# Kernel optimization log

Hardware: AMD Instinct MI355X
Metric: run time of the kernel (lower is better)

Reference implementation:

```python
import math
import jax, jax.numpy as jnp
import numpy as np

TOP_K = 2
_GELU_C = math.sqrt(2.0 / math.pi)

def gelu_new(x):
    # NewGELU: tanh approximation identical to the torch module
    return 0.5 * x * (1.0 + jnp.tanh(_GELU_C * (x + 0.044715 * x * x * x)))

def setup_inputs() -> dict:
    key = jax.random.key(0)
    ks = jax.random.split(key, 6)
    B, T, C, E, H = 2, 2048, 1024, 8, 4096
    s_in = 1.0 / math.sqrt(C)
    s_hid = 1.0 / math.sqrt(H)
    return {
        "x": jax.random.normal(ks[0], (B, T, C), dtype=jnp.float32),
        "router_w": jax.random.normal(ks[1], (E, C), dtype=jnp.float32) * s_in,
        "w_fc": jax.random.normal(ks[2], (E, C, H), dtype=jnp.float32) * s_in,
        "b_fc": jax.random.normal(ks[3], (E, H), dtype=jnp.float32) * 0.02,
        "w_proj": jax.random.normal(ks[4], (E, H, C), dtype=jnp.float32) * s_hid,
        "b_proj": jax.random.normal(ks[5], (E, C), dtype=jnp.float32) * 0.02,
    }

def reference(x, router_w, w_fc, b_fc, w_proj, b_proj):
    B, T, C = x.shape
    E = router_w.shape[0]
    N = B * T
    xf = x.reshape(N, C)
    # Router: Linear(C, E, bias=False), softmax, top-k, renormalize
    logits = xf @ router_w.T                              # [N, E]
    probs = jax.nn.softmax(logits, axis=-1)
    topk_probs, topk_idx = jax.lax.top_k(probs, TOP_K)    # [N, K]
    topk_probs = topk_probs / jnp.sum(topk_probs, axis=-1, keepdims=True)
    # Dense combine weights: zero for unselected experts -> same math as
    # gather/FFN/index_add over selected tokens (dropout=0).
    combine = jnp.zeros((N, E), dtype=x.dtype).at[
        jnp.arange(N)[:, None], topk_idx].add(topk_probs)  # [N, E]
    # Expert FFN applied per expert (batched GEMMs)
    h = gelu_new(jnp.einsum('nc,ech->neh', xf, w_fc) + b_fc)      # [N, E, H]
    out = jnp.einsum('neh,ehc->nec', h, w_proj) + b_proj          # [N, E, C]
    y = jnp.einsum('nec,ne->nc', out, combine)                    # [N, C]
    return y.reshape(B, T, C)
```

## Files before the change

kernel.cpp:

```cpp
#include <hip/hip_runtime.h>


#define NTOK  4096
#define CDIM  1024
#define HDIM  4096
#define NEXP  8
#define NPC   9216
#define MAXMT 72
#define KB_C  32
#define KB_H  128

typedef _Float16 half8 __attribute__((ext_vector_type(8)));
typedef float    f32x4 __attribute__((ext_vector_type(4)));

#define ASYNC_CP16(gp, lp)                                                         \
  __builtin_amdgcn_global_load_lds(                                                \
      (const __attribute__((address_space(1))) unsigned int*)(gp),                 \
      (__attribute__((address_space(3))) unsigned int*)(lp), 16, 0, 0)

#define BAR()     asm volatile("s_barrier" ::: "memory")
#define WAITVM4() asm volatile("s_waitcnt vmcnt(4)" ::: "memory")
#define WAITVM0() asm volatile("s_waitcnt vmcnt(0)" ::: "memory")

__device__ __forceinline__ float gelu_new(float x) {
    const float c = 0.7978845608028654f;
    return 0.5f * x * (1.0f + tanhf(c * (x + 0.044715f * x * x * x)));
}


__global__ void zero_u32(unsigned int* __restrict__ p, int n) {
    int i = blockIdx.x * 256 + threadIdx.x;
    if (i < n) p[i] = 0u;
}

__global__ void zero_meta(unsigned int* __restrict__ pt, unsigned int* __restrict__ pg,
                          unsigned int* __restrict__ cnt) {
    int i = blockIdx.x * 256 + threadIdx.x;
    if (i < NPC) { pt[i] = 0u; pg[i] = 0u; }
    if (i < NEXP) cnt[i] = 0u;
}


__global__ __launch_bounds__(256) void router_kernel(
    const float* __restrict__ x, const float* __restrict__ rw,
    int* __restrict__ tok_e, float* __restrict__ tok_w, int* __restrict__ counts)
{
    int wave = threadIdx.x >> 6, lane = threadIdx.x & 63;
    int n = blockIdx.x * 4 + wave;
    const float* xr = x + (size_t)n * CDIM;
    float acc[NEXP];
    #pragma unroll
    for (int e = 0; e < NEXP; ++e) acc[e] = 0.f;
    for (int c = lane; c < CDIM; c += 64) {
        float xv = xr[c];
        #pragma unroll
        for (int e = 0; e < NEXP; ++e) acc[e] = fmaf(xv, rw[e * CDIM + c], acc[e]);
    }
    #pragma unroll
    for (int e = 0; e < NEXP; ++e) {
        float v = acc[e];
        #pragma unroll
        for (int off = 32; off > 0; off >>= 1) v += __shfl_down(v, off);
        acc[e] = v;
    }
    if (lane == 0) {
        float l0 = -3.0e38f, l1 = -3.0e38f; int b0 = 0, b1 = 0;
        #pragma unroll
        for (int e = 0; e < NEXP; ++e) {
            float v = acc[e];
            if (v > l0)      { l1 = l0; b1 = b0; l0 = v; b0 = e; }
            else if (v > l1) { l1 = v; b1 = e; }
        }
        float t  = expf(l1 - l0);
        float w0 = 1.f / (1.f + t);
        float w1 = t  / (1.f + t);
        tok_e[n * 2]     = b0;  tok_e[n * 2 + 1] = b1;
        tok_w[n * 2]     = w0;  tok_w[n * 2 + 1] = w1;
        atomicAdd(&counts[b0], 1);
        atomicAdd(&counts[b1], 1);
    }
}

__global__ void plan_kernel(const int* __restrict__ counts, int* __restrict__ cursors,
                            int* __restrict__ mtiles, int* __restrict__ tile_expert)
{
    if (threadIdx.x == 0 && blockIdx.x == 0) {
        int b = 0;
        for (int e = 0; e < NEXP; ++e) {
            cursors[e] = b;
            int tiles = (counts[e] + 127) >> 7;
            for (int t = 0; t < tiles; ++t) tile_expert[(b >> 7) + t] = e;
            b += tiles << 7;
        }
        *mtiles = b >> 7;
        for (int t = b >> 7; t < MAXMT; ++t) tile_expert[t] = 0;
    }
}

__global__ void assign_kernel(const int* __restrict__ tok_e, const float* __restrict__ tok_w,
                              int* __restrict__ cursors,
                              int* __restrict__ pair_tok, float* __restrict__ pair_gate)
{
    int n = blockIdx.x * 256 + threadIdx.x;
    #pragma unroll
    for (int k = 0; k < 2; ++k) {
        int e = tok_e[n * 2 + k];
        int slot = atomicAdd(&cursors[e], 1);
        pair_tok[slot]  = n;
        pair_gate[slot] = tok_w[n * 2 + k];
    }
}


__global__ __launch_bounds__(256) void gather_x_kernel(
    const float* __restrict__ x, const int* __restrict__ pair_tok,
    _Float16* __restrict__ xg)
{
    int o = blockIdx.x * 256 + threadIdx.x;
    int kb   = o / (NPC * 4);
    int rem  = o - kb * (NPC * 4);
    int slot = rem >> 2;
    int c    = (rem & 3) * 8;
    int tok  = pair_tok[slot];
    const float* src = x + (size_t)tok * CDIM + kb * 32 + c;
    float4 a = *(const float4*)src;
    float4 b = *(const float4*)(src + 4);
    half8 h;
    h[0] = (_Float16)a.x; h[1] = (_Float16)a.y; h[2] = (_Float16)a.z; h[3] = (_Float16)a.w;
    h[4] = (_Float16)b.x; h[5] = (_Float16)b.y; h[6] = (_Float16)b.z; h[7] = (_Float16)b.w;
    *(half8*)(xg + ((size_t)kb * NPC + slot) * 32 + c) = h;
}


__global__ __launch_bounds__(256) void transpose_cvt_kernel(
    const float* __restrict__ w, _Float16* __restrict__ wt, int K, int N)
{
    __shared__ float tile[32][68];
    const int e = blockIdx.z, k0 = blockIdx.y * 32, n0 = blockIdx.x * 64;
    const float* src = w + ((size_t)e * K + k0) * N + n0;
    const int t = threadIdx.x;
    #pragma unroll
    for (int f = t; f < 512; f += 256) {
        int k = f >> 4, nc = (f & 15) * 4;
        *(float4*)&tile[k][nc] = *(const float4*)(src + (size_t)k * N + nc);
    }
    __syncthreads();
    int n = t >> 2, c2 = (t & 3) * 8;
    half8 h;
    #pragma unroll
    for (int q = 0; q < 8; ++q) h[q] = (_Float16)tile[c2 + q][n];
    int KB = K >> 5;
    _Float16* dst = wt + (((size_t)e * KB + (k0 >> 5)) * N + (n0 + n)) * 32 + c2;
    *(half8*)dst = h;
}


__global__ __launch_bounds__(256, 4) void gemm_fc_kernel(
    const _Float16* __restrict__ xg,
    const _Float16* __restrict__ wt,
    const float*    __restrict__ b_fc,
    const int*      __restrict__ tile_expert,
    const int*      __restrict__ mtiles,
    _Float16*       __restrict__ hb)
{
    const int mt = blockIdx.y;
    if (mt >= *mtiles) return;
    const int nt = blockIdx.x;
    const int e  = tile_expert[mt];
    const int m0 = mt << 7, n0 = nt << 7;

    __shared__ _Float16 As[2][128 * 32];
    __shared__ _Float16 Bs[2][128 * 32];

    const int tid = threadIdx.x;
    const int lane = tid & 63, wv = tid >> 6;
    const int wm = (wv >> 1) * 64, wn = (wv & 1) * 64;
    const int l16 = lane & 15, lq = lane >> 4;

    const char* gA0 = (const char*)xg + (size_t)m0 * 64;
    const char* gB0 = (const char*)wt + ((size_t)e * KB_C * HDIM + n0) * 64;
    const int soff = wv * 2048 + lane * 16;
    char* lA0 = (char*)As[0] + wv * 2048;  char* lA1 = (char*)As[1] + wv * 2048;
    char* lB0 = (char*)Bs[0] + wv * 2048;  char* lB1 = (char*)Bs[1] + wv * 2048;

    f32x4 acc[4][4];
    #pragma unroll
    for (int i = 0; i < 4; ++i)
        #pragma unroll
        for (int j = 0; j < 4; ++j) { acc[i][j][0]=0.f; acc[i][j][1]=0.f; acc[i][j][2]=0.f; acc[i][j][3]=0.f; }

    auto issue = [&](char* lA, char* lB, int kb) {
        const char* ga = gA0 + (size_t)kb * (NPC * 64) + soff;
        const char* gb = gB0 + (size_t)kb * (HDIM * 64) + soff;
        ASYNC_CP16(ga,        lA);
        ASYNC_CP16(ga + 1024, lA + 1024);
        ASYNC_CP16(gb,        lB);
        ASYNC_CP16(gb + 1024, lB + 1024);
    };
    auto compute = [&](const _Float16* Ab, const _Float16* Bb) {
        half8 af[4], bfv[4];
        #pragma unroll
        for (int i = 0; i < 4; ++i) af[i]  = *(const half8*)&Ab[(wm + i * 16 + l16) * 32 + lq * 8];
        #pragma unroll
        for (int j = 0; j < 4; ++j) bfv[j] = *(const half8*)&Bb[(wn + j * 16 + l16) * 32 + lq * 8];
        #pragma unroll
        for (int i = 0; i < 4; ++i)
            #pragma unroll
            for (int j = 0; j < 4; ++j)
                acc[i][j] = __builtin_amdgcn_mfma_f32_16x16x32_f16(af[i], bfv[j], acc[i][j], 0, 0, 0);
    };

    issue(lA0, lB0, 0);
    for (int kb = 0; kb < KB_C; kb += 2) {
        if (kb + 1 < KB_C) { issue(lA1, lB1, kb + 1); WAITVM4(); } else { WAITVM0(); }
        BAR();
        compute(As[0], Bs[0]);
        BAR();
        if (kb + 2 < KB_C) { issue(lA0, lB0, kb + 2); WAITVM4(); } else { WAITVM0(); }
        BAR();
        compute(As[1], Bs[1]);
        BAR();
    }

    float bias[4];
    #pragma unroll
    for (int j = 0; j < 4; ++j) bias[j] = b_fc[e * HDIM + n0 + wn + j * 16 + l16];
    #pragma unroll
    for (int i = 0; i < 4; ++i) {
        #pragma unroll
        for (int r = 0; r < 4; ++r) {
            int slot = m0 + wm + i * 16 + lq * 4 + r;
            #pragma unroll
            for (int j = 0; j < 4; ++j) {
                int n = n0 + wn + j * 16 + l16;
                float v = gelu_new(acc[i][j][r] + bias[j]);
                hb[((size_t)(n >> 5) * NPC + slot) * 32 + (n & 31)] = (_Float16)v;
            }
        }
    }
}


__global__ __launch_bounds__(256, 4) void gemm_proj_kernel(
    const _Float16* __restrict__ hb,
    const _Float16* __restrict__ wt,
    const float*    __restrict__ b_proj,
    const int*      __restrict__ pair_tok,
    const float*    __restrict__ pair_gate,
    const int*      __restrict__ tile_expert,
    const int*      __restrict__ mtiles,
    float*          __restrict__ y)
{
    const int mt = blockIdx.y;
    if (mt >= *mtiles) return;
    const int nt = blockIdx.x;
    const int ks = blockIdx.z;
    const int e  = tile_expert[mt];
    const int m0 = mt << 7, n0 = nt << 7;

    __shared__ _Float16 As[2][128 * 32];
    __shared__ _Float16 Bs[2][128 * 32];

    const int tid = threadIdx.x;
    const int lane = tid & 63, wv = tid >> 6;
    const int wm = (wv >> 1) * 64, wn = (wv & 1) * 64;
    const int l16 = lane & 15, lq = lane >> 4;

    const char* gA0 = (const char*)hb + (size_t)m0 * 64;
    const char* gB0 = (const char*)wt + ((size_t)e * KB_H * CDIM + n0) * 64;
    const int soff = wv * 2048 + lane * 16;
    char* lA0 = (char*)As[0] + wv * 2048;  char* lA1 = (char*)As[1] + wv * 2048;
    char* lB0 = (char*)Bs[0] + wv * 2048;  char* lB1 = (char*)Bs[1] + wv * 2048;

    f32x4 acc[4][4];
    #pragma unroll
    for (int i = 0; i < 4; ++i)
        #pragma unroll
        for (int j = 0; j < 4; ++j) { acc[i][j][0]=0.f; acc[i][j][1]=0.f; acc[i][j][2]=0.f; acc[i][j][3]=0.f; }

    auto issue = [&](char* lA, char* lB, int kb) {
        const char* ga = gA0 + (size_t)kb * (NPC * 64) + soff;
        const char* gb = gB0 + (size_t)kb * (CDIM * 64) + soff;
        ASYNC_CP16(ga,        lA);
        ASYNC_CP16(ga + 1024, lA + 1024);
        ASYNC_CP16(gb,        lB);
        ASYNC_CP16(gb + 1024, lB + 1024);
    };
    auto compute = [&](const _Float16* Ab, const _Float16* Bb) {
        half8 af[4], bfv[4];
        #pragma unroll
        for (int i = 0; i < 4; ++i) af[i]  = *(const half8*)&Ab[(wm + i * 16 + l16) * 32 + lq * 8];
        #pragma unroll
        for (int j = 0; j < 4; ++j) bfv[j] = *(const half8*)&Bb[(wn + j * 16 + l16) * 32 + lq * 8];
        #pragma unroll
        for (int i = 0; i < 4; ++i)
            #pragma unroll
            for (int j = 0; j < 4; ++j)
                acc[i][j] = __builtin_amdgcn_mfma_f32_16x16x32_f16(af[i], bfv[j], acc[i][j], 0, 0, 0);
    };

    const int kbeg = ks * 64, kend = kbeg + 64;
    issue(lA0, lB0, kbeg);
    for (int kb = kbeg; kb < kend; kb += 2) {
        if (kb + 1 < kend) { issue(lA1, lB1, kb + 1); WAITVM4(); } else { WAITVM0(); }
        BAR();
        compute(As[0], Bs[0]);
        BAR();
        if (kb + 2 < kend) { issue(lA0, lB0, kb + 2); WAITVM4(); } else { WAITVM0(); }
        BAR();
        compute(As[1], Bs[1]);
        BAR();
    }

    float bias[4];
    #pragma unroll
    for (int j = 0; j < 4; ++j)
        bias[j] = (ks == 0) ? b_proj[e * CDIM + n0 + wn + j * 16 + l16] : 0.0f;
    #pragma unroll
    for (int i = 0; i < 4; ++i) {
        #pragma unroll
        for (int r = 0; r < 4; ++r) {
            int slot = m0 + wm + i * 16 + lq * 4 + r;
            float g  = pair_gate[slot];
            if (g != 0.0f) {
                int tok = pair_tok[slot];
                float* dst = y + (size_t)tok * CDIM + n0 + wn + l16;
                #pragma unroll
                for (int j = 0; j < 4; ++j)
                    atomicAdd(&dst[j * 16], (acc[i][j][r] + bias[j]) * g);
            }
        }
    }
}


extern "C" void kernel_launch(void* const* d_in, const int* in_sizes, int n_in,
                              void* d_out, int out_size, void* d_ws, size_t ws_size,
                              hipStream_t stream) {
    const float* x   = (const float*)d_in[0];
    const float* rw  = (const float*)d_in[1];
    const float* wfc = (const float*)d_in[2];
    const float* bfc = (const float*)d_in[3];
    const float* wpj = (const float*)d_in[4];
    const float* bpj = (const float*)d_in[5];
    float* y = (float*)d_out;

    char* ws = (char*)d_ws;
    _Float16* xg  = (_Float16*)(ws);
    _Float16* hb  = (_Float16*)(ws + 18874368);
    _Float16* wt  = (_Float16*)(ws + 94371840);
    char* meta = ws + 161480704;
    int*   pair_tok    = (int*)  (meta);
    float* pair_gate   = (float*)(meta + 36864);
    int*   tok_e       = (int*)  (meta + 73728);
    float* tok_w       = (float*)(meta + 106496);
    int*   counts      = (int*)  (meta + 139264);
    int*   cursors     = counts + 8;
    int*   mtiles      = cursors + 8;
    int*   tile_expert = mtiles + 2;

    zero_meta<<<36, 256, 0, stream>>>((unsigned int*)pair_tok, (unsigned int*)pair_gate,
                                      (unsigned int*)counts);
    zero_u32<<<16384, 256, 0, stream>>>((unsigned int*)y, NTOK * CDIM);

    router_kernel<<<1024, 256, 0, stream>>>(x, rw, tok_e, tok_w, counts);
    plan_kernel<<<1, 64, 0, stream>>>(counts, cursors, mtiles, tile_expert);
    assign_kernel<<<16, 256, 0, stream>>>(tok_e, tok_w, cursors, pair_tok, pair_gate);
    gather_x_kernel<<<KB_C * NPC * 4 / 256, 256, 0, stream>>>(x, pair_tok, xg);

    transpose_cvt_kernel<<<dim3(HDIM / 64, CDIM / 32, NEXP), 256, 0, stream>>>(wfc, wt, CDIM, HDIM);
    gemm_fc_kernel<<<dim3(HDIM / 128, MAXMT), 256, 0, stream>>>(
        xg, wt, bfc, tile_expert, mtiles, hb);

    transpose_cvt_kernel<<<dim3(CDIM / 64, HDIM / 32, NEXP), 256, 0, stream>>>(wpj, wt, HDIM, CDIM);
    gemm_proj_kernel<<<dim3(CDIM / 128, MAXMT, 2), 256, 0, stream>>>(
        hb, wt, bpj, pair_tok, pair_gate, tile_expert, mtiles, y);
}
```

Baseline: 736.3 us.

## Use 256x256 GEMM tiles with 512 threads and triple-buffered async loads

```diff
diff --git a/kernel.cpp b/kernel.cpp
--- a/kernel.cpp
+++ b/kernel.cpp
@@ -5,8 +5,8 @@
 #define CDIM  1024
 #define HDIM  4096
 #define NEXP  8
-#define NPC   9216
-#define MAXMT 72
+#define NPC   10240
+#define MAXMT 40
 #define KB_C  32
 #define KB_H  128
 
@@ -19,6 +19,7 @@
       (__attribute__((address_space(3))) unsigned int*)(lp), 16, 0, 0)
 
 #define BAR()     asm volatile("s_barrier" ::: "memory")
+#define WAITVM8() asm volatile("s_waitcnt vmcnt(8)" ::: "memory")
 #define WAITVM4() asm volatile("s_waitcnt vmcnt(4)" ::: "memory")
 #define WAITVM0() asm volatile("s_waitcnt vmcnt(0)" ::: "memory")
 
@@ -88,12 +89,12 @@
         int b = 0;
         for (int e = 0; e < NEXP; ++e) {
             cursors[e] = b;
-            int tiles = (counts[e] + 127) >> 7;
-            for (int t = 0; t < tiles; ++t) tile_expert[(b >> 7) + t] = e;
-            b += tiles << 7;
+            int tiles = (counts[e] + 255) >> 8;
+            for (int t = 0; t < tiles; ++t) tile_expert[(b >> 8) + t] = e;
+            b += tiles << 8;
         }
-        *mtiles = b >> 7;
-        for (int t = b >> 7; t < MAXMT; ++t) tile_expert[t] = 0;
+        *mtiles = b >> 8;
+        for (int t = b >> 8; t < MAXMT; ++t) tile_expert[t] = 0;
     }
 }
 
@@ -155,7 +156,7 @@
 }
 
 
-__global__ __launch_bounds__(256, 4) void gemm_fc_kernel(
+__global__ __launch_bounds__(512, 2) void gemm_fc_kernel(
     const _Float16* __restrict__ xg,
     const _Float16* __restrict__ wt,
     const float*    __restrict__ b_fc,
@@ -167,71 +168,75 @@
     if (mt >= *mtiles) return;
     const int nt = blockIdx.x;
     const int e  = tile_expert[mt];
-    const int m0 = mt << 7, n0 = nt << 7;
-
-    __shared__ _Float16 As[2][128 * 32];
-    __shared__ _Float16 Bs[2][128 * 32];
+    const int m0 = mt << 8, n0 = nt << 8;
+
+    __shared__ _Float16 As[3][256 * 32];
+    __shared__ _Float16 Bs[3][256 * 32];
 
     const int tid = threadIdx.x;
     const int lane = tid & 63, wv = tid >> 6;
-    const int wm = (wv >> 1) * 64, wn = (wv & 1) * 64;
+    const int wm = (wv & 3) * 64, wn = (wv >> 2) * 128;
     const int l16 = lane & 15, lq = lane >> 4;
 
-    const char* gA0 = (const char*)xg + (size_t)m0 * 64;
-    const char* gB0 = (const char*)wt + ((size_t)e * KB_C * HDIM + n0) * 64;
-    const int soff = wv * 2048 + lane * 16;
-    char* lA0 = (char*)As[0] + wv * 2048;  char* lA1 = (char*)As[1] + wv * 2048;
-    char* lB0 = (char*)Bs[0] + wv * 2048;  char* lB1 = (char*)Bs[1] + wv * 2048;
-
-    f32x4 acc[4][4];
+    const int sb = wv >> 2;
+    const int sq = wv & 3;
+    const size_t strideA = (size_t)NPC  * 64;
+    const size_t strideB = (size_t)HDIM * 64;
+    const char* gsrc0 = sb
+        ? (const char*)wt + ((size_t)e * KB_C * HDIM + n0) * 64 + sq * 4096 + lane * 16
+        : (const char*)xg + (size_t)m0 * 64 + sq * 4096 + lane * 16;
+    const size_t gstride = sb ? strideB : strideA;
+
+    f32x4 acc[4][8];
     #pragma unroll
     for (int i = 0; i < 4; ++i)
         #pragma unroll
-        for (int j = 0; j < 4; ++j) { acc[i][j][0]=0.f; acc[i][j][1]=0.f; acc[i][j][2]=0.f; acc[i][j][3]=0.f; }
-
-    auto issue = [&](char* lA, char* lB, int kb) {
-        const char* ga = gA0 + (size_t)kb * (NPC * 64) + soff;
-        const char* gb = gB0 + (size_t)kb * (HDIM * 64) + soff;
-        ASYNC_CP16(ga,        lA);
-        ASYNC_CP16(ga + 1024, lA + 1024);
-        ASYNC_CP16(gb,        lB);
-        ASYNC_CP16(gb + 1024, lB + 1024);
+        for (int j = 0; j < 8; ++j) { acc[i][j][0]=0.f; acc[i][j][1]=0.f; acc[i][j][2]=0.f; acc[i][j][3]=0.f; }
+
+    auto issue = [&](int buf, int kb) {
+        char* ldst = (sb ? (char*)Bs[buf] : (char*)As[buf]) + sq * 4096;
+        const char* g = gsrc0 + (size_t)kb * gstride;
+        ASYNC_CP16(g,        ldst);
+        ASYNC_CP16(g + 1024, ldst + 1024);
+        ASYNC_CP16(g + 2048, ldst + 2048);
+        ASYNC_CP16(g + 3072, ldst + 3072);
     };
     auto compute = [&](const _Float16* Ab, const _Float16* Bb) {
-        half8 af[4], bfv[4];
-        #pragma unroll
-        for (int i = 0; i < 4; ++i) af[i]  = *(const half8*)&Ab[(wm + i * 16 + l16) * 32 + lq * 8];
-        #pragma unroll
-        for (int j = 0; j < 4; ++j) bfv[j] = *(const half8*)&Bb[(wn + j * 16 + l16) * 32 + lq * 8];
+        half8 af[4], bf[8];
+        #pragma unroll
+        for (int i = 0; i < 4; ++i) af[i] = *(const half8*)&Ab[(wm + i * 16 + l16) * 32 + lq * 8];
+        #pragma unroll
+        for (int j = 0; j < 8; ++j) bf[j] = *(const half8*)&Bb[(wn + j * 16 + l16) * 32 + lq * 8];
         #pragma unroll
         for (int i = 0; i < 4; ++i)
             #pragma unroll
-            for (int j = 0; j < 4; ++j)
-                acc[i][j] = __builtin_amdgcn_mfma_f32_16x16x32_f16(af[i], bfv[j], acc[i][j], 0, 0, 0);
+            for (int j = 0; j < 8; ++j)
+                acc[i][j] = __builtin_amdgcn_mfma_f32_16x16x32_f16(af[i], bf[j], acc[i][j], 0, 0, 0);
     };
 
-    issue(lA0, lB0, 0);
-    for (int kb = 0; kb < KB_C; kb += 2) {
-        if (kb + 1 < KB_C) { issue(lA1, lB1, kb + 1); WAITVM4(); } else { WAITVM0(); }
+    issue(0, 0);
+    issue(1, 1);
+    int cur = 0;
+    for (int kb = 0; kb < KB_C; ++kb) {
+        if (kb + 2 < KB_C)      { issue((cur + 2) % 3, kb + 2); WAITVM8(); }
+        else if (kb + 1 < KB_C) { WAITVM4(); }
+        else                    { WAITVM0(); }
         BAR();
-        compute(As[0], Bs[0]);
+        compute(As[cur], Bs[cur]);
         BAR();
-        if (kb + 2 < KB_C) { issue(lA0, lB0, kb + 2); WAITVM4(); } else { WAITVM0(); }
-        BAR();
-        compute(As[1], Bs[1]);
-        BAR();
-    }
-
-    float bias[4];
-    #pragma unroll
-    for (int j = 0; j < 4; ++j) bias[j] = b_fc[e * HDIM + n0 + wn + j * 16 + l16];
+        cur = (cur + 1 == 3) ? 0 : cur + 1;
+    }
+
+    float bias[8];
+    #pragma unroll
+    for (int j = 0; j < 8; ++j) bias[j] = b_fc[e * HDIM + n0 + wn + j * 16 + l16];
     #pragma unroll
     for (int i = 0; i < 4; ++i) {
         #pragma unroll
         for (int r = 0; r < 4; ++r) {
             int slot = m0 + wm + i * 16 + lq * 4 + r;
             #pragma unroll
-            for (int j = 0; j < 4; ++j) {
+            for (int j = 0; j < 8; ++j) {
                 int n = n0 + wn + j * 16 + l16;
                 float v = gelu_new(acc[i][j][r] + bias[j]);
                 hb[((size_t)(n >> 5) * NPC + slot) * 32 + (n & 31)] = (_Float16)v;
@@ -241,7 +246,7 @@
 }
 
 
-__global__ __launch_bounds__(256, 4) void gemm_proj_kernel(
+__global__ __launch_bounds__(512, 2) void gemm_proj_kernel(
     const _Float16* __restrict__ hb,
     const _Float16* __restrict__ wt,
     const float*    __restrict__ b_proj,
@@ -256,65 +261,69 @@
     const int nt = blockIdx.x;
     const int ks = blockIdx.z;
     const int e  = tile_expert[mt];
-    const int m0 = mt << 7, n0 = nt << 7;
-
-    __shared__ _Float16 As[2][128 * 32];
-    __shared__ _Float16 Bs[2][128 * 32];
+    const int m0 = mt << 8, n0 = nt << 8;
+
+    __shared__ _Float16 As[3][256 * 32];
+    __shared__ _Float16 Bs[3][256 * 32];
 
     const int tid = threadIdx.x;
     const int lane = tid & 63, wv = tid >> 6;
-    const int wm = (wv >> 1) * 64, wn = (wv & 1) * 64;
+    const int wm = (wv & 3) * 64, wn = (wv >> 2) * 128;
     const int l16 = lane & 15, lq = lane >> 4;
 
-    const char* gA0 = (const char*)hb + (size_t)m0 * 64;
-    const char* gB0 = (const char*)wt + ((size_t)e * KB_H * CDIM + n0) * 64;
-    const int soff = wv * 2048 + lane * 16;
-    char* lA0 = (char*)As[0] + wv * 2048;  char* lA1 = (char*)As[1] + wv * 2048;
-    char* lB0 = (char*)Bs[0] + wv * 2048;  char* lB1 = (char*)Bs[1] + wv * 2048;
-
-    f32x4 acc[4][4];
+    const int sb = wv >> 2;
+    const int sq = wv & 3;
+    const size_t strideA = (size_t)NPC  * 64;
+    const size_t strideB = (size_t)CDIM * 64;
+    const char* gsrc0 = sb
+        ? (const char*)wt + ((size_t)e * KB_H * CDIM + n0) * 64 + sq * 4096 + lane * 16
+        : (const char*)hb + (size_t)m0 * 64 + sq * 4096 + lane * 16;
+    const size_t gstride = sb ? strideB : strideA;
+
+    f32x4 acc[4][8];
     #pragma unroll
     for (int i = 0; i < 4; ++i)
         #pragma unroll
-        for (int j = 0; j < 4; ++j) { acc[i][j][0]=0.f; acc[i][j][1]=0.f; acc[i][j][2]=0.f; acc[i][j][3]=0.f; }
-
-    auto issue = [&](char* lA, char* lB, int kb) {
-        const char* ga = gA0 + (size_t)kb * (NPC * 64) + soff;
-        const char* gb = gB0 + (size_t)kb * (CDIM * 64) + soff;
-        ASYNC_CP16(ga,        lA);
-        ASYNC_CP16(ga + 1024, lA + 1024);
-        ASYNC_CP16(gb,        lB);
-        ASYNC_CP16(gb + 1024, lB + 1024);
+        for (int j = 0; j < 8; ++j) { acc[i][j][0]=0.f; acc[i][j][1]=0.f; acc[i][j][2]=0.f; acc[i][j][3]=0.f; }
+
+    auto issue = [&](int buf, int kb) {
+        char* ldst = (sb ? (char*)Bs[buf] : (char*)As[buf]) + sq * 4096;
+        const char* g = gsrc0 + (size_t)kb * gstride;
+        ASYNC_CP16(g,        ldst);
+        ASYNC_CP16(g + 1024, ldst + 1024);
+        ASYNC_CP16(g + 2048, ldst + 2048);
+        ASYNC_CP16(g + 3072, ldst + 3072);
     };
     auto compute = [&](const _Float16* Ab, const _Float16* Bb) {
-        half8 af[4], bfv[4];
-        #pragma unroll
-        for (int i = 0; i < 4; ++i) af[i]  = *(const half8*)&Ab[(wm + i * 16 + l16) * 32 + lq * 8];
-        #pragma unroll
-        for (int j = 0; j < 4; ++j) bfv[j] = *(const half8*)&Bb[(wn + j * 16 + l16) * 32 + lq * 8];
+        half8 af[4], bf[8];
+        #pragma unroll
+        for (int i = 0; i < 4; ++i) af[i] = *(const half8*)&Ab[(wm + i * 16 + l16) * 32 + lq * 8];
+        #pragma unroll
+        for (int j = 0; j < 8; ++j) bf[j] = *(const half8*)&Bb[(wn + j * 16 + l16) * 32 + lq * 8];
         #pragma unroll
         for (int i = 0; i < 4; ++i)
             #pragma unroll
-            for (int j = 0; j < 4; ++j)
-                acc[i][j] = __builtin_amdgcn_mfma_f32_16x16x32_f16(af[i], bfv[j], acc[i][j], 0, 0, 0);
+            for (int j = 0; j < 8; ++j)
+                acc[i][j] = __builtin_amdgcn_mfma_f32_16x16x32_f16(af[i], bf[j], acc[i][j], 0, 0, 0);
     };
 
-    const int kbeg = ks * 64, kend = kbeg + 64;
-    issue(lA0, lB0, kbeg);
-    for (int kb = kbeg; kb < kend; kb += 2) {
-        if (kb + 1 < kend) { issue(lA1, lB1, kb + 1); WAITVM4(); } else { WAITVM0(); }
+    const int kbeg = ks * 32, kend = kbeg + 32;
+    issue(0, kbeg);
+    issue(1, kbeg + 1);
+    int cur = 0;
+    for (int kb = kbeg; kb < kend; ++kb) {
+        if (kb + 2 < kend)      { issue((cur + 2) % 3, kb + 2); WAITVM8(); }
+        else if (kb + 1 < kend) { WAITVM4(); }
+        else                    { WAITVM0(); }
         BAR();
-        compute(As[0], Bs[0]);
+        compute(As[cur], Bs[cur]);
         BAR();
-        if (kb + 2 < kend) { issue(lA0, lB0, kb + 2); WAITVM4(); } else { WAITVM0(); }
-        BAR();
-        compute(As[1], Bs[1]);
-        BAR();
-    }
-
-    float bias[4];
-    #pragma unroll
-    for (int j = 0; j < 4; ++j)
+        cur = (cur + 1 == 3) ? 0 : cur + 1;
+    }
+
+    float bias[8];
+    #pragma unroll
+    for (int j = 0; j < 8; ++j)
         bias[j] = (ks == 0) ? b_proj[e * CDIM + n0 + wn + j * 16 + l16] : 0.0f;
     #pragma unroll
     for (int i = 0; i < 4; ++i) {
@@ -326,7 +335,7 @@
                 int tok = pair_tok[slot];
                 float* dst = y + (size_t)tok * CDIM + n0 + wn + l16;
                 #pragma unroll
-                for (int j = 0; j < 4; ++j)
+                for (int j = 0; j < 8; ++j)
                     atomicAdd(&dst[j * 16], (acc[i][j][r] + bias[j]) * g);
             }
         }
@@ -347,19 +356,19 @@
 
     char* ws = (char*)d_ws;
     _Float16* xg  = (_Float16*)(ws);
-    _Float16* hb  = (_Float16*)(ws + 18874368);
-    _Float16* wt  = (_Float16*)(ws + 94371840);
-    char* meta = ws + 161480704;
+    _Float16* hb  = (_Float16*)(ws + 20971520);
+    _Float16* wt  = (_Float16*)(ws + 104857600);
+    char* meta = ws + 171966464;
     int*   pair_tok    = (int*)  (meta);
-    float* pair_gate   = (float*)(meta + 36864);
-    int*   tok_e       = (int*)  (meta + 73728);
-    float* tok_w       = (float*)(meta + 106496);
-    int*   counts      = (int*)  (meta + 139264);
+    float* pair_gate   = (float*)(meta + 40960);
+    int*   tok_e       = (int*)  (meta + 81920);
+    float* tok_w       = (float*)(meta + 114688);
+    int*   counts      = (int*)  (meta + 147456);
     int*   cursors     = counts + 8;
     int*   mtiles      = cursors + 8;
     int*   tile_expert = mtiles + 2;
 
-    zero_meta<<<36, 256, 0, stream>>>((unsigned int*)pair_tok, (unsigned int*)pair_gate,
+    zero_meta<<<40, 256, 0, stream>>>((unsigned int*)pair_tok, (unsigned int*)pair_gate,
                                       (unsigned int*)counts);
     zero_u32<<<16384, 256, 0, stream>>>((unsigned int*)y, NTOK * CDIM);
 
@@ -369,10 +378,10 @@
     gather_x_kernel<<<KB_C * NPC * 4 / 256, 256, 0, stream>>>(x, pair_tok, xg);
 
     transpose_cvt_kernel<<<dim3(HDIM / 64, CDIM / 32, NEXP), 256, 0, stream>>>(wfc, wt, CDIM, HDIM);
-    gemm_fc_kernel<<<dim3(HDIM / 128, MAXMT), 256, 0, stream>>>(
+    gemm_fc_kernel<<<dim3(HDIM / 256, MAXMT), 512, 0, stream>>>(
         xg, wt, bfc, tile_expert, mtiles, hb);
 
     transpose_cvt_kernel<<<dim3(CDIM / 64, HDIM / 32, NEXP), 256, 0, stream>>>(wpj, wt, HDIM, CDIM);
-    gemm_proj_kernel<<<dim3(CDIM / 128, MAXMT, 2), 256, 0, stream>>>(
+    gemm_proj_kernel<<<dim3(CDIM / 256, MAXMT, 4), 512, 0, stream>>>(
         hb, wt, bpj, pair_tok, pair_gate, tile_expert, mtiles, y);
 }
```

Measured after the change: 762.9 us. +3.6%, slower.
